# Optimization experiments

Measured on AMD Instinct MI355X. Metric: run time of the kernel, lower is better.

## Reference

```python
import jax, jax.numpy as jnp
import numpy as np

DIM = 112; WIN = 8; DIM_HEAD = 28; HEADS = DIM // DIM_HEAD; DH = DIM_HEAD // 2
B_SPEC = 8; H = 128; W = 128; BATCH = 2; NTOK = WIN * WIN


def _conv3d_grouped(x, w, groups):
    # x: [N, C, D, H, W], w: [O, C//groups, kD, kH, kW]
    return jax.lax.conv_general_dilated(
        x, w, window_strides=(1, 1, 1), padding='SAME',
        feature_group_count=groups,
        dimension_numbers=('NCDHW', 'OIDHW', 'NCDHW'))


def setup_inputs() -> dict:
    key = jax.random.key(0)
    ks = jax.random.split(key, 13)
    g = DIM // 2
    x = jax.random.normal(ks[0], (BATCH, DIM, B_SPEC, H, W), jnp.float32)
    last = jax.random.normal(ks[1], (BATCH, DIM, B_SPEC, H, W), jnp.float32)
    s3 = 1.0 / np.sqrt(2 * 27)  # fan_in of grouped 3x3x3 conv (2 in-ch per group)
    Wq = jax.random.normal(ks[2], (g, 2, 3, 3, 3), jnp.float32) * s3
    Wk = jax.random.normal(ks[3], (g, 2, 3, 3, 3), jnp.float32) * s3
    Wv = jax.random.normal(ks[4], (g, 2, 3, 3, 3), jnp.float32) * s3
    Wout = jax.random.normal(ks[5], (DIM, 1, 1, 1, 1), jnp.float32)
    pcq_w = jax.random.normal(ks[6], (1, DH), jnp.float32) / np.sqrt(DH)
    pcq_b = jnp.ones((1,), jnp.float32)
    pck_w = jax.random.normal(ks[7], (1, DH), jnp.float32) / np.sqrt(DH)
    pck_b = jnp.ones((1,), jnp.float32)
    mlp1_w = jax.random.normal(ks[8], (1, NTOK), jnp.float32) / np.sqrt(NTOK)
    mlp2_w1 = jax.random.normal(ks[9], (NTOK, NTOK), jnp.float32) / np.sqrt(NTOK)
    mlp2_w2 = jax.random.normal(ks[10], (1, NTOK), jnp.float32) / np.sqrt(NTOK)
    return dict(x=x, last=last, Wq=Wq, Wk=Wk, Wv=Wv, Wout=Wout,
                pcq_w=pcq_w, pcq_b=pcq_b, pck_w=pck_w, pck_b=pck_b,
                mlp1_w=mlp1_w, mlp2_w1=mlp2_w1, mlp2_w2=mlp2_w2)


def _win_heads(t, b, g, Bs, nh, nw):
    # [b, g, B, H, W] -> [(b nh nw), heads, B, ntok, d]
    t = t.reshape(b, g, Bs, nh, WIN, nw, WIN)
    t = t.transpose(0, 3, 5, 4, 6, 2, 1)  # b, nh, nw, b0, b1, B, c
    t = t.reshape(b * nh * nw, NTOK, Bs, g)
    t = t.reshape(b * nh * nw, NTOK, Bs, HEADS, g // HEADS)
    return t.transpose(0, 3, 2, 1, 4)  # bp, h, B, n, d


def reference(x, last, Wq, Wk, Wv, Wout, pcq_w, pcq_b, pck_w, pck_b,
              mlp1_w, mlp2_w1, mlp2_w2):
    b, c, Bs, Hh, Ww = x.shape
    g = c // 2
    nh, nw = Hh // WIN, Ww // WIN
    q = _conv3d_grouped(x, Wq, g)
    k = _conv3d_grouped(last, Wk, g)
    v = _conv3d_grouped(last, Wv, g)
    qh = _win_heads(q, b, g, Bs, nh, nw)
    kh = _win_heads(k, b, g, Bs, nh, nw)
    vh = _win_heads(v, b, g, Bs, nh, nw)
    # Sigma projections: Linear(d,1) + scalar bias
    Sq = jnp.einsum('bhBnd,od->bhBno', qh, pcq_w) + pcq_b  # [bp,h,B,n,1]
    Sk = jnp.einsum('bhBnd,od->bhBno', kh, pck_w) + pck_b
    sim = jnp.einsum('bhBid,bhBjd->bhBij', qh, kh)
    Sigma = Sq * jnp.swapaxes(Sk, -1, -2)  # outer product over the size-1 dim
    eye = jnp.eye(NTOK, dtype=sim.dtype)
    sim_norm = sim * (1.0 - eye)  # remove diagonal
    t1 = jnp.einsum('bhBij,oj->bhBio', sim_norm, mlp1_w)[..., 0]  # [bp,h,B,n]
    t2 = jax.nn.leaky_relu(jnp.einsum('bhBi,oi->bhBo', t1, mlp2_w1), 0.1)
    theta = jnp.einsum('bhBi,oi->bhBo', t2, mlp2_w2)[..., None]  # [bp,h,B,1,1]
    sims = sim * Sigma
    attn = jax.nn.softmax(sims, axis=-1) * (sims > theta).astype(sims.dtype)
    out = jnp.einsum('bhBij,bhBjd->bhBid', attn, vh)
    # merge heads -> [(b nh nw), n, B, c]
    out = out.transpose(0, 3, 2, 1, 4).reshape(b * nh * nw, NTOK, Bs, g)
    # windows back to image: b, c, B, H, W
    out = out.reshape(b, nh, nw, WIN, WIN, Bs, g)
    out = out.transpose(0, 6, 5, 1, 3, 2, 4).reshape(b, g, Bs, Hh, Ww)
    return _conv3d_grouped(out, Wout, g)
```

## Files before the change

### kernel.cpp

```cpp
#include <hip/hip_runtime.h>
#include <math.h>

#define XCH 112
#define GCH 56
#define BS  8
#define HH  128
#define WW  128
#define CHS (BS*HH*WW)
#define HW  (HH*WW)
#define DD  14

__global__ __launch_bounds__(256) void conv_qkv_kernel(
    const float* __restrict__ x, const float* __restrict__ last,
    const float* __restrict__ Wq, const float* __restrict__ Wk,
    const float* __restrict__ Wv,
    float* __restrict__ qws, float* __restrict__ kws, float* __restrict__ vws)
{
    __shared__ float wq[54], wk[54], wv[54];
    const int tid = threadIdx.x;
    const int go = blockIdx.y;
    const int b  = blockIdx.z;
    if (tid < 54)        wq[tid]      = Wq[go*54 + tid];
    else if (tid < 108)  wk[tid-54]   = Wk[go*54 + (tid-54)];
    else if (tid < 162)  wv[tid-108]  = Wv[go*54 + (tid-108)];
    __syncthreads();

    const int xx = tid & 127;
    const int y  = blockIdx.x*2 + (tid >> 7);

    float accq[8], acck[8], accv[8];
    #pragma unroll
    for (int d = 0; d < 8; ++d) { accq[d] = 0.f; acck[d] = 0.f; accv[d] = 0.f; }

    #pragma unroll
    for (int ci = 0; ci < 2; ++ci) {
        const float* bx = x    + (size_t)(b*XCH + go*2 + ci)*CHS;
        const float* bl = last + (size_t)(b*XCH + go*2 + ci)*CHS;
        #pragma unroll
        for (int ky = 0; ky < 3; ++ky) {
            const int yy = y + ky - 1;
            const bool yok = ((unsigned)yy < (unsigned)HH);
            #pragma unroll
            for (int kx = 0; kx < 3; ++kx) {
                const int xx2 = xx + kx - 1;
                const bool ok = yok && ((unsigned)xx2 < (unsigned)WW);
                const int off = yy*WW + xx2;
                float cx[8], cl[8];
                #pragma unroll
                for (int z = 0; z < 8; ++z) {
                    cx[z] = ok ? bx[z*HW + off] : 0.f;
                    cl[z] = ok ? bl[z*HW + off] : 0.f;
                }
                #pragma unroll
                for (int kd = 0; kd < 3; ++kd) {
                    const int wi = ci*27 + kd*9 + ky*3 + kx;
                    const float wqv = wq[wi];
                    const float wkv = wk[wi];
                    const float wvv = wv[wi];
                    #pragma unroll
                    for (int d = 0; d < 8; ++d) {
                        const int z = d + kd - 1;
                        if (z >= 0 && z < 8) {
                            accq[d] = fmaf(cx[z], wqv, accq[d]);
                            acck[d] = fmaf(cl[z], wkv, acck[d]);
                            accv[d] = fmaf(cl[z], wvv, accv[d]);
                        }
                    }
                }
            }
        }
    }
    const size_t obase = (size_t)(b*GCH + go)*CHS + (size_t)y*WW + xx;
    #pragma unroll
    for (int d = 0; d < 8; ++d) {
        qws[obase + (size_t)d*HW] = accq[d];
        kws[obase + (size_t)d*HW] = acck[d];
        vws[obase + (size_t)d*HW] = accv[d];
    }
}

__global__ __launch_bounds__(256) void attn_kernel(
    const float* __restrict__ qws, const float* __restrict__ kws,
    const float* __restrict__ vws,
    const float* __restrict__ pcq_w, const float* __restrict__ pcq_b,
    const float* __restrict__ pck_w, const float* __restrict__ pck_b,
    const float* __restrict__ mlp1_w, const float* __restrict__ mlp2_w1,
    const float* __restrict__ mlp2_w2, const float* __restrict__ Wout,
    float* __restrict__ out)
{
    __shared__ __align__(16) float kv[4][2][64][16];
    __shared__ float w1T[64*65];
    __shared__ float t1s[4][64];
    __shared__ float m2w2[64];
    __shared__ float woutS[112];
    __shared__ float pcqS[14], pckS[14];

    const int tid = threadIdx.x;
    for (int idx = tid; idx < 4096; idx += 256) {
        const int o = idx >> 6, i = idx & 63;
        w1T[i*65 + o] = mlp2_w1[idx];
    }
    if (tid < 64)  m2w2[tid]  = mlp2_w2[tid];
    if (tid < 112) woutS[tid] = Wout[tid];
    if (tid < 14)  { pcqS[tid] = pcq_w[tid]; pckS[tid] = pck_w[tid]; }
    __syncthreads();

    const float bq = pcq_b[0];
    const float bk = pck_b[0];

    const int head = blockIdx.x & 3;
    const int bp   = blockIdx.x >> 2;
    const int wx   = bp & 15;
    const int wy   = (bp >> 4) & 15;
    const int b    = bp >> 8;

    const int wave = tid >> 6;
    const int lane = tid & 63;
    const int iy = lane >> 3, ix = lane & 7;
    const int y = wy*8 + iy, x = wx*8 + ix;

    float (*kl)[16] = kv[wave][0];
    float (*vl)[16] = kv[wave][1];

    for (int d_ = wave; d_ < 8; d_ += 4) {
        const size_t spat = (size_t)d_*HW + (size_t)y*WW + x;
        const size_t cb = (size_t)(b*GCH + head*DD)*CHS + spat;

        float qr[14], kr[14], vr[14];
        #pragma unroll
        for (int dd = 0; dd < 14; ++dd) {
            qr[dd] = qws[cb + (size_t)dd*CHS];
            kr[dd] = kws[cb + (size_t)dd*CHS];
            vr[dd] = vws[cb + (size_t)dd*CHS];
        }
        float Sq = bq, Sk = bk, diag = 0.f;
        #pragma unroll
        for (int dd = 0; dd < 14; ++dd) {
            Sq   = fmaf(qr[dd], pcqS[dd], Sq);
            Sk   = fmaf(kr[dd], pckS[dd], Sk);
            diag = fmaf(qr[dd], kr[dd], diag);
        }
        const float m1own = mlp1_w[lane];

        float4* krow = (float4*)&kl[lane][0];
        krow[0] = make_float4(kr[0], kr[1], kr[2],  kr[3]);
        krow[1] = make_float4(kr[4], kr[5], kr[6],  kr[7]);
        krow[2] = make_float4(kr[8], kr[9], kr[10], kr[11]);
        krow[3] = make_float4(kr[12], kr[13], Sk,   m1own);
        float4* vrow = (float4*)&vl[lane][0];
        vrow[0] = make_float4(vr[0], vr[1], vr[2],  vr[3]);
        vrow[1] = make_float4(vr[4], vr[5], vr[6],  vr[7]);
        vrow[2] = make_float4(vr[8], vr[9], vr[10], vr[11]);
        vrow[3] = make_float4(vr[12], vr[13], 0.f,  0.f);

        float sims[64];
        float rmax = -1e30f;
        float t1 = 0.f;
        #pragma unroll
        for (int j = 0; j < 64; ++j) {
            const float* kp = &kl[j][0];
            const float4 a0 = *(const float4*)(kp);
            const float4 a1 = *(const float4*)(kp + 4);
            const float4 a2 = *(const float4*)(kp + 8);
            const float4 a3 = *(const float4*)(kp + 12);
            float s = qr[0]*a0.x;
            s = fmaf(qr[1],  a0.y, s); s = fmaf(qr[2],  a0.z, s);
            s = fmaf(qr[3],  a0.w, s); s = fmaf(qr[4],  a1.x, s);
            s = fmaf(qr[5],  a1.y, s); s = fmaf(qr[6],  a1.z, s);
            s = fmaf(qr[7],  a1.w, s); s = fmaf(qr[8],  a2.x, s);
            s = fmaf(qr[9],  a2.y, s); s = fmaf(qr[10], a2.z, s);
            s = fmaf(qr[11], a2.w, s); s = fmaf(qr[12], a3.x, s);
            s = fmaf(qr[13], a3.y, s);
            t1 = fmaf(s, a3.w, t1);
            const float sv = s * Sq * a3.z;
            sims[j] = sv;
            rmax = fmaxf(rmax, sv);
        }
        t1 = fmaf(-diag, m1own, t1);

        t1s[wave][lane] = t1;
        float t2 = 0.f;
        #pragma unroll
        for (int i = 0; i < 64; ++i)
            t2 = fmaf(t1s[wave][i], w1T[i*65 + lane], t2);
        t2 = (t2 > 0.f) ? t2 : 0.1f*t2;
        float th = t2 * m2w2[lane];
        #pragma unroll
        for (int m = 32; m >= 1; m >>= 1)
            th += __shfl_xor(th, m, 64);

        float denom = 0.f;
        float acc[14];
        #pragma unroll
        for (int dd = 0; dd < 14; ++dd) acc[dd] = 0.f;
        #pragma unroll
        for (int j = 0; j < 64; ++j) {
            const float sv = sims[j];
            const float e = __expf(sv - rmax);
            denom += e;
            const float a = (sv > th) ? e : 0.f;
            const float* vp = &vl[j][0];
            const float4 b0 = *(const float4*)(vp);
            const float4 b1 = *(const float4*)(vp + 4);
            const float4 b2 = *(const float4*)(vp + 8);
            const float4 b3 = *(const float4*)(vp + 12);
            acc[0]  = fmaf(a, b0.x, acc[0]);  acc[1]  = fmaf(a, b0.y, acc[1]);
            acc[2]  = fmaf(a, b0.z, acc[2]);  acc[3]  = fmaf(a, b0.w, acc[3]);
            acc[4]  = fmaf(a, b1.x, acc[4]);  acc[5]  = fmaf(a, b1.y, acc[5]);
            acc[6]  = fmaf(a, b1.z, acc[6]);  acc[7]  = fmaf(a, b1.w, acc[7]);
            acc[8]  = fmaf(a, b2.x, acc[8]);  acc[9]  = fmaf(a, b2.y, acc[9]);
            acc[10] = fmaf(a, b2.z, acc[10]); acc[11] = fmaf(a, b2.w, acc[11]);
            acc[12] = fmaf(a, b3.x, acc[12]); acc[13] = fmaf(a, b3.y, acc[13]);
        }
        const float inv = 1.0f / denom;

        #pragma unroll
        for (int dd = 0; dd < 14; ++dd) {
            const float val = acc[dd] * inv;
            const int c = head*DD + dd;
            const size_t o0 = (size_t)(b*XCH + 2*c)*CHS + spat;
            out[o0]       = val * woutS[2*c];
            out[o0 + CHS] = val * woutS[2*c + 1];
        }
    }
}

extern "C" void kernel_launch(void* const* d_in, const int* in_sizes, int n_in,
                              void* d_out, int out_size, void* d_ws, size_t ws_size,
                              hipStream_t stream) {
    const float* x       = (const float*)d_in[0];
    const float* last    = (const float*)d_in[1];
    const float* Wq      = (const float*)d_in[2];
    const float* Wk      = (const float*)d_in[3];
    const float* Wv      = (const float*)d_in[4];
    const float* Wout    = (const float*)d_in[5];
    const float* pcq_w   = (const float*)d_in[6];
    const float* pcq_b   = (const float*)d_in[7];
    const float* pck_w   = (const float*)d_in[8];
    const float* pck_b   = (const float*)d_in[9];
    const float* mlp1_w  = (const float*)d_in[10];
    const float* mlp2_w1 = (const float*)d_in[11];
    const float* mlp2_w2 = (const float*)d_in[12];
    float* out = (float*)d_out;

    const size_t tsz = (size_t)2*GCH*CHS;
    float* qws = (float*)d_ws;
    float* kws = qws + tsz;
    float* vws = kws + tsz;

    conv_qkv_kernel<<<dim3(64, 56, 2), 256, 0, stream>>>(
        x, last, Wq, Wk, Wv, qws, kws, vws);
    attn_kernel<<<dim3(512*4), 256, 0, stream>>>(
        qws, kws, vws, pcq_w, pcq_b, pck_w, pck_b,
        mlp1_w, mlp2_w1, mlp2_w2, Wout, out);
}
```

Baseline: 922.6 us.

## Stage conv halo tiles in LDS and recompute attention scores instead of storing

The conv kernel now loads a halo tile of both input volumes into shared memory once per input channel and reads all 27 taps from LDS instead of issuing repeated global loads. The attention kernel drops the 64-entry sims register array and recomputes the q·k dot products in the second pass, cutting register pressure so launch bounds can ask for more waves per SIMD. The w1T padding is also removed. The trade-off is extra LDS traffic and syncs in the conv kernel, plus duplicated FMAs in attention, and removing the padding may add bank conflicts on the transpose store.

```diff
diff --git a/kernel.cpp b/kernel.cpp
--- a/kernel.cpp
+++ b/kernel.cpp
@@ -10,46 +10,57 @@
 #define HW  (HH*WW)
 #define DD  14
 
-__global__ __launch_bounds__(256) void conv_qkv_kernel(
+__global__ __launch_bounds__(256, 4) void conv_qkv_kernel(
     const float* __restrict__ x, const float* __restrict__ last,
     const float* __restrict__ Wq, const float* __restrict__ Wk,
     const float* __restrict__ Wv,
     float* __restrict__ qws, float* __restrict__ kws, float* __restrict__ vws)
 {
     __shared__ float wq[54], wk[54], wv[54];
+    __shared__ float stage[2][8][4][132];
+
     const int tid = threadIdx.x;
     const int go = blockIdx.y;
     const int b  = blockIdx.z;
     if (tid < 54)        wq[tid]      = Wq[go*54 + tid];
     else if (tid < 108)  wk[tid-54]   = Wk[go*54 + (tid-54)];
     else if (tid < 162)  wv[tid-108]  = Wv[go*54 + (tid-108)];
-    __syncthreads();
 
     const int xx = tid & 127;
-    const int y  = blockIdx.x*2 + (tid >> 7);
+    const int ty = tid >> 7;
+    const int y0 = blockIdx.x*2;
 
     float accq[8], acck[8], accv[8];
     #pragma unroll
     for (int d = 0; d < 8; ++d) { accq[d] = 0.f; acck[d] = 0.f; accv[d] = 0.f; }
 
-    #pragma unroll
     for (int ci = 0; ci < 2; ++ci) {
+        __syncthreads();
         const float* bx = x    + (size_t)(b*XCH + go*2 + ci)*CHS;
         const float* bl = last + (size_t)(b*XCH + go*2 + ci)*CHS;
+        for (int idx = tid; idx < 8320; idx += 256) {
+            const int t = (idx >= 4160) ? 1 : 0;
+            int rem = idx - t*4160;
+            const int z = rem / 520;  rem -= z*520;
+            const int r = rem / 130;
+            const int c = rem - r*130;
+            const int yy = y0 - 1 + r;
+            const int xg = c - 1;
+            float v = 0.f;
+            if ((unsigned)yy < 128u && (unsigned)xg < 128u)
+                v = (t ? bl : bx)[z*HW + yy*WW + xg];
+            stage[t][z][r][c] = v;
+        }
+        __syncthreads();
         #pragma unroll
         for (int ky = 0; ky < 3; ++ky) {
-            const int yy = y + ky - 1;
-            const bool yok = ((unsigned)yy < (unsigned)HH);
             #pragma unroll
             for (int kx = 0; kx < 3; ++kx) {
-                const int xx2 = xx + kx - 1;
-                const bool ok = yok && ((unsigned)xx2 < (unsigned)WW);
-                const int off = yy*WW + xx2;
                 float cx[8], cl[8];
                 #pragma unroll
                 for (int z = 0; z < 8; ++z) {
-                    cx[z] = ok ? bx[z*HW + off] : 0.f;
-                    cl[z] = ok ? bl[z*HW + off] : 0.f;
+                    cx[z] = stage[0][z][ty+ky][xx+kx];
+                    cl[z] = stage[1][z][ty+ky][xx+kx];
                 }
                 #pragma unroll
                 for (int kd = 0; kd < 3; ++kd) {
@@ -70,6 +81,7 @@
             }
         }
     }
+    const int y = y0 + ty;
     const size_t obase = (size_t)(b*GCH + go)*CHS + (size_t)y*WW + xx;
     #pragma unroll
     for (int d = 0; d < 8; ++d) {
@@ -79,7 +91,7 @@
     }
 }
 
-__global__ __launch_bounds__(256) void attn_kernel(
+__global__ __launch_bounds__(256, 3) void attn_kernel(
     const float* __restrict__ qws, const float* __restrict__ kws,
     const float* __restrict__ vws,
     const float* __restrict__ pcq_w, const float* __restrict__ pcq_b,
@@ -89,17 +101,15 @@
     float* __restrict__ out)
 {
     __shared__ __align__(16) float kv[4][2][64][16];
-    __shared__ float w1T[64*65];
+    __shared__ float w1T[4096];
     __shared__ float t1s[4][64];
     __shared__ float m2w2[64];
     __shared__ float woutS[112];
     __shared__ float pcqS[14], pckS[14];
 
     const int tid = threadIdx.x;
-    for (int idx = tid; idx < 4096; idx += 256) {
-        const int o = idx >> 6, i = idx & 63;
-        w1T[i*65 + o] = mlp2_w1[idx];
-    }
+    for (int idx = tid; idx < 4096; idx += 256)
+        w1T[(idx & 63)*64 + (idx >> 6)] = mlp2_w1[idx];
     if (tid < 64)  m2w2[tid]  = mlp2_w2[tid];
     if (tid < 112) woutS[tid] = Wout[tid];
     if (tid < 14)  { pcqS[tid] = pcq_w[tid]; pckS[tid] = pck_w[tid]; }
@@ -153,7 +163,6 @@
         vrow[2] = make_float4(vr[8], vr[9], vr[10], vr[11]);
         vrow[3] = make_float4(vr[12], vr[13], 0.f,  0.f);
 
-        float sims[64];
         float rmax = -1e30f;
         float t1 = 0.f;
         #pragma unroll
@@ -173,7 +182,6 @@
             s = fmaf(qr[13], a3.y, s);
             t1 = fmaf(s, a3.w, t1);
             const float sv = s * Sq * a3.z;
-            sims[j] = sv;
             rmax = fmaxf(rmax, sv);
         }
         t1 = fmaf(-diag, m1own, t1);
@@ -182,7 +190,7 @@
         float t2 = 0.f;
         #pragma unroll
         for (int i = 0; i < 64; ++i)
-            t2 = fmaf(t1s[wave][i], w1T[i*65 + lane], t2);
+            t2 = fmaf(t1s[wave][i], w1T[i*64 + lane], t2);
         t2 = (t2 > 0.f) ? t2 : 0.1f*t2;
         float th = t2 * m2w2[lane];
         #pragma unroll
@@ -195,7 +203,20 @@
         for (int dd = 0; dd < 14; ++dd) acc[dd] = 0.f;
         #pragma unroll
         for (int j = 0; j < 64; ++j) {
-            const float sv = sims[j];
+            const float* kp = &kl[j][0];
+            const float4 a0 = *(const float4*)(kp);
+            const float4 a1 = *(const float4*)(kp + 4);
+            const float4 a2 = *(const float4*)(kp + 8);
+            const float4 a3 = *(const float4*)(kp + 12);
+            float s = qr[0]*a0.x;
+            s = fmaf(qr[1],  a0.y, s); s = fmaf(qr[2],  a0.z, s);
+            s = fmaf(qr[3],  a0.w, s); s = fmaf(qr[4],  a1.x, s);
+            s = fmaf(qr[5],  a1.y, s); s = fmaf(qr[6],  a1.z, s);
+            s = fmaf(qr[7],  a1.w, s); s = fmaf(qr[8],  a2.x, s);
+            s = fmaf(qr[9],  a2.y, s); s = fmaf(qr[10], a2.z, s);
+            s = fmaf(qr[11], a2.w, s); s = fmaf(qr[12], a3.x, s);
+            s = fmaf(qr[13], a3.y, s);
+            const float sv = s * Sq * a3.z;
             const float e = __expf(sv - rmax);
             denom += e;
             const float a = (sv > th) ? e : 0.f;
```

Result: slower. 2.405 ms (+160.7%).
